# Optimization experiments

Hardware: AMD Instinct MI355X
Metric: run time of the kernel (lower is better)

Reference implementation:

```python
import jax, jax.numpy as jnp
import numpy as np

B, Q, D, H, HD, P = 1, 2048, 2048, 16, 128, 512


def setup_inputs() -> dict:
    key = jax.random.key(0)
    ks = jax.random.split(key, 12)
    x = jax.random.normal(ks[0], (B, Q, D), jnp.float32)
    prefix_key = jax.random.normal(ks[1], (B, P, H, HD), jnp.float32)
    prefix_value = jax.random.normal(ks[2], (B, P, H, HD), jnp.float32)
    s = 1.0 / np.sqrt(D)
    Wq = jax.random.normal(ks[3], (D, H, HD), jnp.float32) * s
    Wk = jax.random.normal(ks[4], (D, H, HD), jnp.float32) * s
    Wv = jax.random.normal(ks[5], (D, H, HD), jnp.float32) * s
    bq = jnp.zeros((H, HD), jnp.float32)
    bk = jnp.zeros((H, HD), jnp.float32)
    bv = jnp.zeros((H, HD), jnp.float32)
    prefix_gate = jax.random.normal(ks[6], (H,), jnp.float32) * 0.1
    Wout = jax.random.normal(ks[7], (H, HD, D), jnp.float32) * (1.0 / np.sqrt(D))
    bout = jnp.zeros((D,), jnp.float32)
    # prefix fully visible, causal mask over the suffix (current sequence)
    causal = jnp.tril(jnp.ones((Q, Q), bool))
    mask = jnp.concatenate([jnp.ones((Q, P), bool), causal], axis=1)[None, None]  # [1,1,Q,P+Q]
    return dict(x=x, prefix_key=prefix_key, prefix_value=prefix_value,
                Wq=Wq, bq=bq, Wk=Wk, bk=bk, Wv=Wv, bv=bv,
                prefix_gate=prefix_gate, Wout=Wout, bout=bout, mask=mask)


def reference(x, prefix_key, prefix_value, Wq, bq, Wk, bk, Wv, bv, prefix_gate, Wout, bout, mask):
    head_dim = Wq.shape[-1]
    pl = prefix_key.shape[1]
    q = jnp.einsum('bqd,dhk->bqhk', x, Wq) + bq   # [B,Q,H,HD]
    k = jnp.einsum('bqd,dhk->bqhk', x, Wk) + bk
    v = jnp.einsum('bqd,dhk->bqhk', x, Wv) + bv
    k = jnp.concatenate([prefix_key, k], axis=1)   # [B,P+Q,H,HD]
    v = jnp.concatenate([prefix_value, v], axis=1)
    q = q / jnp.sqrt(jnp.asarray(head_dim, q.dtype))
    w = jnp.einsum('bqhd,bkhd->bhqk', q, k)        # [B,H,Q,P+Q]
    big_neg = jnp.finfo(w.dtype).min
    w = jnp.where(mask, w, big_neg)
    gate = prefix_gate[None, :, None, None]
    w_prefix = jax.nn.softmax(w[..., :pl]) * gate   # gated prefix segment
    w_suffix = jax.nn.softmax(w[..., pl:])          # regular suffix softmax
    w = jnp.concatenate([w_prefix, w_suffix], axis=-1)
    o = jnp.einsum('bhqk,bkhd->bqhd', w, v)         # [B,Q,H,HD]
    return jnp.einsum('bqhd,hdo->bqo', o, Wout) + bout
```

## Files before the change

### kernel.cpp

```cpp
#include <hip/hip_runtime.h>
#include <hip/hip_bf16.h>

typedef __bf16 bf16x8 __attribute__((ext_vector_type(8)));
typedef __bf16 bf16x4v __attribute__((ext_vector_type(4)));
typedef float f32x4 __attribute__((ext_vector_type(4)));

#define DMODEL 2048
#define NH 16
#define HD 128
#define PLEN 512
#define QLEN 2048
#define KVLEN 2560

__device__ __forceinline__ void gload_lds16(const void* g, void* l) {
  __builtin_amdgcn_global_load_lds((const __attribute__((address_space(1))) void*)g,
                                   (__attribute__((address_space(3))) void*)l, 16, 0, 0);
}


__global__ __launch_bounds__(256) void k_transpose4(const float* __restrict__ s0,
                                                    const float* __restrict__ s1,
                                                    const float* __restrict__ s2,
                                                    const float* __restrict__ s3,
                                                    __bf16* __restrict__ d0,
                                                    __bf16* __restrict__ d1,
                                                    __bf16* __restrict__ d2,
                                                    __bf16* __restrict__ d3) {
  __shared__ float tile[64][65];
  const int z = blockIdx.z;
  const float* in = (z == 0) ? s0 : (z == 1) ? s1 : (z == 2) ? s2 : s3;
  __bf16* out = (z == 0) ? d0 : (z == 1) ? d1 : (z == 2) ? d2 : d3;
  const int t = threadIdx.x;
  const int tx = t & 63, ty = t >> 6;
  const int r0 = blockIdx.y * 64, c0 = blockIdx.x * 64;
#pragma unroll
  for (int i = 0; i < 16; ++i) {
    int r = ty + i * 4;
    tile[r][tx] = in[(size_t)(r0 + r) * DMODEL + c0 + tx];
  }
  __syncthreads();
#pragma unroll
  for (int i = 0; i < 16; ++i) {
    int r = ty + i * 4;
    out[(size_t)(c0 + r) * DMODEL + r0 + tx] = (__bf16)tile[tx][r];
  }
}

__global__ __launch_bounds__(256) void k_f32_to_bf16(const float* __restrict__ in,
                                                     __bf16* __restrict__ out, int n4) {
  int i = blockIdx.x * blockDim.x + threadIdx.x;
  int stride = gridDim.x * blockDim.x;
  for (; i < n4; i += stride) {
    float4 v = ((const float4*)in)[i];
    bf16x4v o;
    o[0] = (__bf16)v.x; o[1] = (__bf16)v.y; o[2] = (__bf16)v.z; o[3] = (__bf16)v.w;
    ((bf16x4v*)out)[i] = o;
  }
}

__global__ __launch_bounds__(256) void k_prefix(const float* __restrict__ pk,
                                                const float* __restrict__ pv,
                                                __bf16* __restrict__ Kall,
                                                __bf16* __restrict__ VT) {
  int idx = blockIdx.x * 256 + threadIdx.x;
  int hd = idx & 127;
  int h = (idx >> 7) & 15;
  int p = idx >> 11;
  Kall[(size_t)h * KVLEN * HD + (size_t)p * HD + hd] = (__bf16)pk[idx];
  VT[(size_t)h * HD * KVLEN + (size_t)hd * KVLEN + p] = (__bf16)pv[idx];
}


template <int BN>
__device__ __forceinline__ void stage_tile(const __bf16* __restrict__ A,
                                           const __bf16* __restrict__ BT,
                                           char* AsmB, char* BsmB,
                                           int m0, int n0, int k0, int w, int l) {
#pragma unroll
  for (int i = 0; i < 2; ++i) {
    int base = i * 4096 + w * 1024;
    int o = base + l * 16;
    int row = o >> 6, col = (o & 63) >> 1;
    gload_lds16(A + (size_t)(m0 + row) * DMODEL + k0 + col, AsmB + base);
  }
  if constexpr (BN == 128) {
#pragma unroll
    for (int i = 0; i < 2; ++i) {
      int base = i * 4096 + w * 1024;
      int o = base + l * 16;
      int row = o >> 6, col = (o & 63) >> 1;
      gload_lds16(BT + (size_t)(n0 + row) * DMODEL + k0 + col, BsmB + base);
    }
  } else {
    int base = w * 1024;
    int o = base + l * 16;
    int row = o >> 6, col = (o & 63) >> 1;
    gload_lds16(BT + (size_t)(n0 + row) * DMODEL + k0 + col, BsmB + base);
  }
}

template <int BN>
__device__ __forceinline__ void gemm_mainloop_db(const __bf16* __restrict__ A,
                                                 const __bf16* __restrict__ BT,
                                                 __bf16* Asm, __bf16* Bsm,
                                                 int m0, int n0, int w, int l,
                                                 f32x4 (&acc)[4][BN / 32]) {
  constexpr int NI = BN / 32;
  constexpr int ABUF = 4096;
  constexpr int BBUF = BN * 32;
  const int lr = l & 15, lg = l >> 4;
  int cur = 0;
  stage_tile<BN>(A, BT, (char*)Asm, (char*)Bsm, m0, n0, 0, w, l);
  __syncthreads();
  for (int k0 = 0; k0 < DMODEL; k0 += 32) {
    if (k0 + 32 < DMODEL)
      stage_tile<BN>(A, BT, (char*)(Asm + (cur ^ 1) * ABUF), (char*)(Bsm + (cur ^ 1) * BBUF),
                     m0, n0, k0 + 32, w, l);
    const __bf16* Ab = Asm + cur * ABUF;
    const __bf16* Bb = Bsm + cur * BBUF;
    bf16x8 af[4], bfv[NI];
#pragma unroll
    for (int mi = 0; mi < 4; ++mi)
      af[mi] = *(const bf16x8*)(Ab + ((w >> 1) * 64 + mi * 16 + lr) * 32 + lg * 8);
#pragma unroll
    for (int ni = 0; ni < NI; ++ni)
      bfv[ni] = *(const bf16x8*)(Bb + ((w & 1) * (BN / 2) + ni * 16 + lr) * 32 + lg * 8);
    __builtin_amdgcn_s_setprio(1);
#pragma unroll
    for (int mi = 0; mi < 4; ++mi)
#pragma unroll
      for (int ni = 0; ni < NI; ++ni)
        acc[mi][ni] = __builtin_amdgcn_mfma_f32_16x16x32_bf16(af[mi], bfv[ni], acc[mi][ni], 0, 0, 0);
    __builtin_amdgcn_s_setprio(0);
    __syncthreads();
    cur ^= 1;
  }
}

__global__ __launch_bounds__(256) void gemm_qkv(const __bf16* __restrict__ xb,
                                                const __bf16* __restrict__ WqT,
                                                const __bf16* __restrict__ WkT,
                                                const __bf16* __restrict__ WvT,
                                                const float* __restrict__ bq,
                                                const float* __restrict__ bk,
                                                const float* __restrict__ bv,
                                                __bf16* __restrict__ Qs,
                                                __bf16* __restrict__ Kall,
                                                __bf16* __restrict__ VT) {
  __shared__ __bf16 Asm[2][4096];
  __shared__ __bf16 Bsm[2][4096];
  const int t = threadIdx.x, w = t >> 6, l = t & 63;
  const int m0 = blockIdx.x * 128, n0 = blockIdx.y * 128;
  const int z = blockIdx.z;
  const __bf16* BT = (z == 0) ? WqT : ((z == 1) ? WkT : WvT);
  const float* bias = (z == 0) ? bq : ((z == 1) ? bk : bv);
  f32x4 acc[4][4];
#pragma unroll
  for (int mi = 0; mi < 4; ++mi)
#pragma unroll
    for (int ni = 0; ni < 4; ++ni) acc[mi][ni] = (f32x4){0.f, 0.f, 0.f, 0.f};
  gemm_mainloop_db<128>(xb, BT, &Asm[0][0], &Bsm[0][0], m0, n0, w, l, acc);
  const int lr = l & 15, lg = l >> 4;
#pragma unroll
  for (int mi = 0; mi < 4; ++mi)
#pragma unroll
    for (int ni = 0; ni < 4; ++ni)
#pragma unroll
      for (int r = 0; r < 4; ++r) {
        int row = m0 + (w >> 1) * 64 + mi * 16 + lg * 4 + r;
        int col = n0 + (w & 1) * 64 + ni * 16 + lr;
        float v = acc[mi][ni][r] + bias[col];
        int hh = col >> 7, hd = col & 127;
        if (z == 0) {
          Qs[(size_t)hh * QLEN * HD + (size_t)row * HD + hd] = (__bf16)(v * 0.08838834764831845f);
        } else if (z == 1) {
          Kall[(size_t)hh * KVLEN * HD + (size_t)(PLEN + row) * HD + hd] = (__bf16)v;
        } else {
          VT[(size_t)hh * HD * KVLEN + (size_t)hd * KVLEN + (PLEN + row)] = (__bf16)v;
        }
      }
}

__global__ __launch_bounds__(256) void gemm_out(const __bf16* __restrict__ Ob,
                                                const __bf16* __restrict__ WoT,
                                                const float* __restrict__ bout,
                                                float* __restrict__ out) {
  __shared__ __bf16 Asm[2][4096];
  __shared__ __bf16 Bsm[2][2048];
  const int t = threadIdx.x, w = t >> 6, l = t & 63;
  const int m0 = blockIdx.x * 128, n0 = blockIdx.y * 64;
  f32x4 acc[4][2];
#pragma unroll
  for (int mi = 0; mi < 4; ++mi)
#pragma unroll
    for (int ni = 0; ni < 2; ++ni) acc[mi][ni] = (f32x4){0.f, 0.f, 0.f, 0.f};
  gemm_mainloop_db<64>(Ob, WoT, &Asm[0][0], &Bsm[0][0], m0, n0, w, l, acc);
  const int lr = l & 15, lg = l >> 4;
#pragma unroll
  for (int mi = 0; mi < 4; ++mi)
#pragma unroll
    for (int ni = 0; ni < 2; ++ni)
#pragma unroll
      for (int r = 0; r < 4; ++r) {
        int row = m0 + (w >> 1) * 64 + mi * 16 + lg * 4 + r;
        int col = n0 + (w & 1) * 32 + ni * 16 + lr;
        out[(size_t)row * DMODEL + col] = acc[mi][ni][r] + bout[col];
      }
}

template <int KS>
__global__ __launch_bounds__(256, 4) void k_attn(const __bf16* __restrict__ Qs,
                                                 const __bf16* __restrict__ Kall,
                                                 const __bf16* __restrict__ VT,
                                                 __bf16* __restrict__ P1buf,
                                                 float* __restrict__ S1buf,
                                                 __bf16* __restrict__ P2buf,
                                                 float* __restrict__ S2buf) {
  __shared__ __bf16 Ksm[2][4096];
  __shared__ __bf16 Vsm[2][4096];
  __shared__ __bf16 Pl[4][16 * 40];
  const int id = blockIdx.x;
  const int b = id & 255, k = id >> 8;
  const int h = b >> 4, m = b & 15;
  int qt, z;
  if constexpr (KS == 2) {
    z = k >> 1;
    const int j = 2 * m + (k >> 1);
    qt = (k & 1) ? (31 - j) : j;
  } else {
    z = 0;
    qt = (k & 1) ? (31 - 2 * m) : (2 * m);
  }
  const int t = threadIdx.x, w = t >> 6, l = t & 63;
  const int lr = l & 15, lg = l >> 4;
  const int q0 = qt * 64 + w * 16;
  const __bf16* Qh = Qs + (size_t)h * QLEN * HD;
  const char* Khb = (const char*)(Kall + (size_t)h * KVLEN * HD);
  const char* Vhb = (const char*)(VT + (size_t)h * HD * KVLEN);
  __bf16* Pw = &Pl[w][0];

  bf16x8 qf[4];
#pragma unroll
  for (int c = 0; c < 4; ++c)
    qf[c] = *(const bf16x8*)(Qh + (size_t)(q0 + lr) * HD + c * 32 + lg * 8);

  f32x4 acc[8];
  float ss[4];

  auto STAGE = [&](int buf, int kb) {
#pragma unroll
    for (int i = 0; i < 2; ++i) {
      int o = (i * 256 + w * 64 + l) * 16;
      int po = o ^ (((o >> 8) & 7) << 4);
      gload_lds16(Khb + (size_t)kb * 256 + po, (char*)&Ksm[buf][0] + i * 4096 + w * 1024);
    }
#pragma unroll
    for (int i = 0; i < 2; ++i) {
      int o = (i * 256 + w * 64 + l) * 16;
      int po = o ^ (((o >> 7) & 7) << 4);
      int row = po >> 6, colb = po & 63;
      gload_lds16(Vhb + (size_t)row * (KVLEN * 2) + (size_t)kb * 2 + colb,
                  (char*)&Vsm[buf][0] + i * 4096 + w * 1024);
    }
  };

  auto COMPUTE = [&](int buf, int mrel, bool domask) {
    const char* Kb = (const char*)&Ksm[buf][0];
    const char* Vb = (const char*)&Vsm[buf][0];
    f32x4 st0 = {0.f, 0.f, 0.f, 0.f}, st1 = {0.f, 0.f, 0.f, 0.f};
    __builtin_amdgcn_s_setprio(1);
#pragma unroll
    for (int c = 0; c < 4; ++c) {
      int o0 = lr * 256 + c * 64 + lg * 16;        o0 ^= ((o0 >> 8) & 7) << 4;
      int o1 = (16 + lr) * 256 + c * 64 + lg * 16; o1 ^= ((o1 >> 8) & 7) << 4;
      bf16x8 kf0 = *(const bf16x8*)(Kb + o0);
      bf16x8 kf1 = *(const bf16x8*)(Kb + o1);
      st0 = __builtin_amdgcn_mfma_f32_16x16x32_bf16(qf[c], kf0, st0, 0, 0, 0);
      st1 = __builtin_amdgcn_mfma_f32_16x16x32_bf16(qf[c], kf1, st1, 0, 0, 0);
    }
    __builtin_amdgcn_s_setprio(0);
#pragma unroll
    for (int r = 0; r < 4; ++r) {
      if (domask) {
        int qq = q0 + lg * 4 + r;
        if (mrel + lr > qq) st0[r] = -1e30f;
        if (mrel + 16 + lr > qq) st1[r] = -1e30f;
      }
      float p0 = __expf(st0[r] - 16.0f);
      float p1 = __expf(st1[r] - 16.0f);
      ss[r] += p0 + p1;
      Pw[(lg * 4 + r) * 40 + lr] = (__bf16)p0;
      Pw[(lg * 4 + r) * 40 + 16 + lr] = (__bf16)p1;
    }
    bf16x8 pf = *(const bf16x8*)(Pw + lr * 40 + lg * 8);
    __builtin_amdgcn_s_setprio(1);
#pragma unroll
    for (int c = 0; c < 8; ++c) {
      int o = (c * 16 + lr) * 64 + lg * 16; o ^= ((o >> 7) & 7) << 4;
      bf16x8 vf = *(const bf16x8*)(Vb + o);
      acc[c] = __builtin_amdgcn_mfma_f32_16x16x32_bf16(pf, vf, acc[c], 0, 0, 0);
    }
    __builtin_amdgcn_s_setprio(0);
  };

  auto STORE_PHASE = [&](__bf16* PBUF, float* SBUF) {
    const size_t rb = (size_t)(z * NH + h) * QLEN;
#pragma unroll
    for (int r = 0; r < 4; ++r) {
      float s = ss[r];
      s += __shfl_xor(s, 1); s += __shfl_xor(s, 2);
      s += __shfl_xor(s, 4); s += __shfl_xor(s, 8);
      const int row = q0 + lg * 4 + r;
      if (lr == 0) SBUF[rb + row] = s;
#pragma unroll
      for (int c = 0; c < 8; ++c)
        PBUF[(rb + row) * HD + c * 16 + lr] = (__bf16)acc[c][r];
    }
  };

#pragma unroll
  for (int c = 0; c < 8; ++c) acc[c] = (f32x4){0.f, 0.f, 0.f, 0.f};
#pragma unroll
  for (int r = 0; r < 4; ++r) ss[r] = 0.f;
  int cur = 0;
  STAGE(0, z * 32);
  __syncthreads();
#pragma unroll 1
  for (int tt = z; tt < 16; tt += KS) {
    if (tt + KS < 16) STAGE(cur ^ 1, (tt + KS) * 32);
    else STAGE(cur ^ 1, PLEN + z * 32);
    COMPUTE(cur, 0, false);
    __syncthreads();
    cur ^= 1;
  }
  STORE_PHASE(P1buf, S1buf);

#pragma unroll
  for (int c = 0; c < 8; ++c) acc[c] = (f32x4){0.f, 0.f, 0.f, 0.f};
#pragma unroll
  for (int r = 0; r < 4; ++r) ss[r] = 0.f;
  const int ntb = 2 * qt + 2;
#pragma unroll 1
  for (int tt = z; tt < ntb; tt += KS) {
    if (tt + KS < ntb) STAGE(cur ^ 1, PLEN + (tt + KS) * 32);
    COMPUTE(cur, tt * 32, tt * 32 + 31 > q0);
    __syncthreads();
    cur ^= 1;
  }
  STORE_PHASE(P2buf, S2buf);
}

template <int KS>
__global__ __launch_bounds__(256) void k_combine(const __bf16* __restrict__ P1buf,
                                                 const float* __restrict__ S1buf,
                                                 const __bf16* __restrict__ P2buf,
                                                 const float* __restrict__ S2buf,
                                                 const float* __restrict__ gate,
                                                 __bf16* __restrict__ Ob) {
  const int idx = blockIdx.x * 256 + threadIdx.x;
  const int d = idx & 127;
  const int q = (idx >> 7) & 2047;
  const int h = idx >> 18;
  const size_t rq = (size_t)h * QLEN + q;
  float a1 = 0.f, a2 = 0.f, s1 = 0.f, s2 = 0.f;
#pragma unroll
  for (int zz = 0; zz < KS; ++zz) {
    const size_t zb = (size_t)zz * NH * QLEN;
    a1 += (float)P1buf[(zb + rq) * HD + d];
    a2 += (float)P2buf[(zb + rq) * HD + d];
    s1 += S1buf[zb + rq];
    s2 += S2buf[zb + rq];
  }
  float o = a1 * (gate[h] / s1) + a2 / s2;
  Ob[(size_t)q * DMODEL + h * HD + d] = (__bf16)o;
}


extern "C" void kernel_launch(void* const* d_in, const int* in_sizes, int n_in,
                              void* d_out, int out_size, void* d_ws, size_t ws_size,
                              hipStream_t stream) {
  const float* x    = (const float*)d_in[0];
  const float* pk   = (const float*)d_in[1];
  const float* pv   = (const float*)d_in[2];
  const float* Wq   = (const float*)d_in[3];
  const float* bq   = (const float*)d_in[4];
  const float* Wk   = (const float*)d_in[5];
  const float* bk   = (const float*)d_in[6];
  const float* Wv   = (const float*)d_in[7];
  const float* bv   = (const float*)d_in[8];
  const float* gate = (const float*)d_in[9];
  const float* Wout = (const float*)d_in[10];
  const float* bout = (const float*)d_in[11];
  float* out = (float*)d_out;

  char* ws = (char*)d_ws;
  size_t off = 0;
  auto alc = [&](size_t bytes) -> char* {
    char* p = ws + off;
    off += bytes;
    off = (off + 255) & ~(size_t)255;
    return p;
  };
  __bf16* xb   = (__bf16*)alc((size_t)DMODEL * DMODEL * 2);
  __bf16* WqT  = (__bf16*)alc((size_t)DMODEL * DMODEL * 2);
  __bf16* WkT  = (__bf16*)alc((size_t)DMODEL * DMODEL * 2);
  __bf16* WvT  = (__bf16*)alc((size_t)DMODEL * DMODEL * 2);
  __bf16* WoT  = (__bf16*)alc((size_t)DMODEL * DMODEL * 2);
  __bf16* Qs   = (__bf16*)alc((size_t)NH * QLEN * HD * 2);
  __bf16* Kall = (__bf16*)alc((size_t)NH * KVLEN * HD * 2);
  __bf16* VTa  = (__bf16*)alc((size_t)NH * HD * KVLEN * 2);
  __bf16* Ob   = (__bf16*)alc((size_t)QLEN * DMODEL * 2);

  const size_t per_split = (size_t)NH * QLEN * HD * 2 * 2
                         + (size_t)NH * QLEN * 4 * 2 + 1024;
  int KS = (off + 2 * per_split <= ws_size) ? 2 : 1;
  __bf16* P1buf = (__bf16*)alc((size_t)KS * NH * QLEN * HD * 2);
  __bf16* P2buf = (__bf16*)alc((size_t)KS * NH * QLEN * HD * 2);
  float*  S1buf = (float*)alc((size_t)KS * NH * QLEN * 4);
  float*  S2buf = (float*)alc((size_t)KS * NH * QLEN * 4);

  k_transpose4<<<dim3(32, 32, 4), 256, 0, stream>>>(Wq, Wk, Wv, Wout, WqT, WkT, WvT, WoT);
  k_f32_to_bf16<<<1024, 256, 0, stream>>>(x, xb, (DMODEL * DMODEL) / 4);
  k_prefix<<<4096, 256, 0, stream>>>(pk, pv, Kall, VTa);

  gemm_qkv<<<dim3(16, 16, 3), 256, 0, stream>>>(xb, WqT, WkT, WvT, bq, bk, bv, Qs, Kall, VTa);

  const int ncomb = (NH * QLEN * HD) / 256;
  if (KS == 2) {
    k_attn<2><<<1024, 256, 0, stream>>>(Qs, Kall, VTa, P1buf, S1buf, P2buf, S2buf);
    k_combine<2><<<ncomb, 256, 0, stream>>>(P1buf, S1buf, P2buf, S2buf, gate, Ob);
  } else {
    k_attn<1><<<512, 256, 0, stream>>>(Qs, Kall, VTa, P1buf, S1buf, P2buf, S2buf);
    k_combine<1><<<ncomb, 256, 0, stream>>>(P1buf, S1buf, P2buf, S2buf, gate, Ob);
  }
  gemm_out<<<dim3(16, 32), 256, 0, stream>>>(Ob, WoT, bout, out);
}
```

Baseline: 195.0 us.

## Fuse prep kernels and keep attention probabilities in registers via transposed QK MFMA

Merges the weight transpose, x conversion and prefix K/V layout kernels into one launch, which removes two kernel launches and their serialization. In the attention kernel the QK^T MFMA operands are swapped so scores arrive transposed. The probability tile is then built with packed bf16 conversion and lane shuffles instead of a round trip through shared memory. The row-sum reduction also shrinks to a single scalar per lane. This removes LDS traffic and per-row shuffle reductions but adds shuffles and selects, and the shuffle index math must exactly match the MFMA operand layout.

```diff
diff --git a/kernel.cpp b/kernel.cpp
--- a/kernel.cpp
+++ b/kernel.cpp
@@ -17,57 +17,64 @@
                                    (__attribute__((address_space(3))) void*)l, 16, 0, 0);
 }
 
-
-__global__ __launch_bounds__(256) void k_transpose4(const float* __restrict__ s0,
-                                                    const float* __restrict__ s1,
-                                                    const float* __restrict__ s2,
-                                                    const float* __restrict__ s3,
-                                                    __bf16* __restrict__ d0,
-                                                    __bf16* __restrict__ d1,
-                                                    __bf16* __restrict__ d2,
-                                                    __bf16* __restrict__ d3) {
+__device__ __forceinline__ unsigned cvt_pk_bf16(float lo, float hi) {
+  unsigned r;
+  asm volatile("v_cvt_pk_bf16_f32 %0, %1, %2" : "=v"(r) : "v"(lo), "v"(hi));
+  return r;
+}
+
+__global__ __launch_bounds__(256) void k_prep(const float* __restrict__ Wq,
+                                              const float* __restrict__ Wk,
+                                              const float* __restrict__ Wv,
+                                              const float* __restrict__ Wo,
+                                              const float* __restrict__ x,
+                                              const float* __restrict__ pk,
+                                              const float* __restrict__ pv,
+                                              __bf16* __restrict__ WqT,
+                                              __bf16* __restrict__ WkT,
+                                              __bf16* __restrict__ WvT,
+                                              __bf16* __restrict__ WoT,
+                                              __bf16* __restrict__ xb,
+                                              __bf16* __restrict__ Kall,
+                                              __bf16* __restrict__ VT) {
   __shared__ float tile[64][65];
   const int z = blockIdx.z;
-  const float* in = (z == 0) ? s0 : (z == 1) ? s1 : (z == 2) ? s2 : s3;
-  __bf16* out = (z == 0) ? d0 : (z == 1) ? d1 : (z == 2) ? d2 : d3;
   const int t = threadIdx.x;
   const int tx = t & 63, ty = t >> 6;
-  const int r0 = blockIdx.y * 64, c0 = blockIdx.x * 64;
-#pragma unroll
-  for (int i = 0; i < 16; ++i) {
-    int r = ty + i * 4;
-    tile[r][tx] = in[(size_t)(r0 + r) * DMODEL + c0 + tx];
-  }
-  __syncthreads();
-#pragma unroll
-  for (int i = 0; i < 16; ++i) {
-    int r = ty + i * 4;
-    out[(size_t)(c0 + r) * DMODEL + r0 + tx] = (__bf16)tile[tx][r];
-  }
-}
-
-__global__ __launch_bounds__(256) void k_f32_to_bf16(const float* __restrict__ in,
-                                                     __bf16* __restrict__ out, int n4) {
-  int i = blockIdx.x * blockDim.x + threadIdx.x;
-  int stride = gridDim.x * blockDim.x;
-  for (; i < n4; i += stride) {
-    float4 v = ((const float4*)in)[i];
-    bf16x4v o;
-    o[0] = (__bf16)v.x; o[1] = (__bf16)v.y; o[2] = (__bf16)v.z; o[3] = (__bf16)v.w;
-    ((bf16x4v*)out)[i] = o;
-  }
-}
-
-__global__ __launch_bounds__(256) void k_prefix(const float* __restrict__ pk,
-                                                const float* __restrict__ pv,
-                                                __bf16* __restrict__ Kall,
-                                                __bf16* __restrict__ VT) {
-  int idx = blockIdx.x * 256 + threadIdx.x;
-  int hd = idx & 127;
-  int h = (idx >> 7) & 15;
-  int p = idx >> 11;
-  Kall[(size_t)h * KVLEN * HD + (size_t)p * HD + hd] = (__bf16)pk[idx];
-  VT[(size_t)h * HD * KVLEN + (size_t)hd * KVLEN + p] = (__bf16)pv[idx];
+  if (z < 4) {
+    const float* in = (z == 0) ? Wq : (z == 1) ? Wk : (z == 2) ? Wv : Wo;
+    __bf16* out = (z == 0) ? WqT : (z == 1) ? WkT : (z == 2) ? WvT : WoT;
+    const int r0 = blockIdx.y * 64, c0 = blockIdx.x * 64;
+#pragma unroll
+    for (int i = 0; i < 16; ++i) {
+      int r = ty + i * 4;
+      tile[r][tx] = in[(size_t)(r0 + r) * DMODEL + c0 + tx];
+    }
+    __syncthreads();
+#pragma unroll
+    for (int i = 0; i < 16; ++i) {
+      int r = ty + i * 4;
+      out[(size_t)(c0 + r) * DMODEL + r0 + tx] = (__bf16)tile[tx][r];
+    }
+  } else if (z == 4) {
+    const int r0 = blockIdx.y * 64, c0 = blockIdx.x * 64;
+#pragma unroll
+    for (int i = 0; i < 16; ++i) {
+      int r = ty + i * 4;
+      xb[(size_t)(r0 + r) * DMODEL + c0 + tx] = (__bf16)x[(size_t)(r0 + r) * DMODEL + c0 + tx];
+    }
+  } else {
+    const int blk = blockIdx.y * 32 + blockIdx.x;
+#pragma unroll
+    for (int i = 0; i < 4; ++i) {
+      int idx = blk * 1024 + i * 256 + t;
+      int hd = idx & 127;
+      int hh = (idx >> 7) & 15;
+      int p = idx >> 11;
+      Kall[(size_t)hh * KVLEN * HD + (size_t)p * HD + hd] = (__bf16)pk[idx];
+      VT[(size_t)hh * HD * KVLEN + (size_t)hd * KVLEN + p] = (__bf16)pv[idx];
+    }
+  }
 }
 
 
@@ -218,7 +225,6 @@
                                                  float* __restrict__ S2buf) {
   __shared__ __bf16 Ksm[2][4096];
   __shared__ __bf16 Vsm[2][4096];
-  __shared__ __bf16 Pl[4][16 * 40];
   const int id = blockIdx.x;
   const int b = id & 255, k = id >> 8;
   const int h = b >> 4, m = b & 15;
@@ -237,7 +243,6 @@
   const __bf16* Qh = Qs + (size_t)h * QLEN * HD;
   const char* Khb = (const char*)(Kall + (size_t)h * KVLEN * HD);
   const char* Vhb = (const char*)(VT + (size_t)h * HD * KVLEN);
-  __bf16* Pw = &Pl[w][0];
 
   bf16x8 qf[4];
 #pragma unroll
@@ -245,7 +250,7 @@
     qf[c] = *(const bf16x8*)(Qh + (size_t)(q0 + lr) * HD + c * 32 + lg * 8);
 
   f32x4 acc[8];
-  float ss[4];
+  float ss;
 
   auto STAGE = [&](int buf, int kb) {
 #pragma unroll
@@ -275,24 +280,40 @@
       int o1 = (16 + lr) * 256 + c * 64 + lg * 16; o1 ^= ((o1 >> 8) & 7) << 4;
       bf16x8 kf0 = *(const bf16x8*)(Kb + o0);
       bf16x8 kf1 = *(const bf16x8*)(Kb + o1);
-      st0 = __builtin_amdgcn_mfma_f32_16x16x32_bf16(qf[c], kf0, st0, 0, 0, 0);
-      st1 = __builtin_amdgcn_mfma_f32_16x16x32_bf16(qf[c], kf1, st1, 0, 0, 0);
+      st0 = __builtin_amdgcn_mfma_f32_16x16x32_bf16(kf0, qf[c], st0, 0, 0, 0);
+      st1 = __builtin_amdgcn_mfma_f32_16x16x32_bf16(kf1, qf[c], st1, 0, 0, 0);
     }
     __builtin_amdgcn_s_setprio(0);
+    const int qabs = q0 + lr;
+    float e0[4], e1[4];
+    float ps = 0.f;
 #pragma unroll
     for (int r = 0; r < 4; ++r) {
+      e0[r] = __expf(st0[r] - 16.0f);
+      e1[r] = __expf(st1[r] - 16.0f);
       if (domask) {
-        int qq = q0 + lg * 4 + r;
-        if (mrel + lr > qq) st0[r] = -1e30f;
-        if (mrel + 16 + lr > qq) st1[r] = -1e30f;
+        if (mrel + 4 * lg + r > qabs) e0[r] = 0.f;
+        if (mrel + 16 + 4 * lg + r > qabs) e1[r] = 0.f;
       }
-      float p0 = __expf(st0[r] - 16.0f);
-      float p1 = __expf(st1[r] - 16.0f);
-      ss[r] += p0 + p1;
-      Pw[(lg * 4 + r) * 40 + lr] = (__bf16)p0;
-      Pw[(lg * 4 + r) * 40 + 16 + lr] = (__bf16)p1;
-    }
-    bf16x8 pf = *(const bf16x8*)(Pw + lr * 40 + lg * 8);
+      ps += e0[r] + e1[r];
+    }
+    ss += ps;
+    unsigned W0 = cvt_pk_bf16(e0[0], e0[1]);
+    unsigned W1 = cvt_pk_bf16(e0[2], e0[3]);
+    unsigned W2 = cvt_pk_bf16(e1[0], e1[1]);
+    unsigned W3 = cvt_pk_bf16(e1[2], e1[3]);
+    const int srcA = lr + (((2 * lg) & 3) << 4);
+    const int srcB = lr + (((2 * lg + 1) & 3) << 4);
+    unsigned A0 = __shfl(W0, srcA), A1 = __shfl(W1, srcA);
+    unsigned A2 = __shfl(W0, srcB), A3 = __shfl(W1, srcB);
+    unsigned B0 = __shfl(W2, srcA), B1 = __shfl(W3, srcA);
+    unsigned B2 = __shfl(W2, srcB), B3 = __shfl(W3, srcB);
+    union { unsigned u[4]; bf16x8 v; } pu;
+    pu.u[0] = (lg < 2) ? A0 : B0;
+    pu.u[1] = (lg < 2) ? A1 : B1;
+    pu.u[2] = (lg < 2) ? A2 : B2;
+    pu.u[3] = (lg < 2) ? A3 : B3;
+    bf16x8 pf = pu.v;
     __builtin_amdgcn_s_setprio(1);
 #pragma unroll
     for (int c = 0; c < 8; ++c) {
@@ -305,13 +326,13 @@
 
   auto STORE_PHASE = [&](__bf16* PBUF, float* SBUF) {
     const size_t rb = (size_t)(z * NH + h) * QLEN;
+    float s = ss;
+    s += __shfl_xor(s, 16);
+    s += __shfl_xor(s, 32);
+    if (l < 16) SBUF[rb + q0 + l] = s;
 #pragma unroll
     for (int r = 0; r < 4; ++r) {
-      float s = ss[r];
-      s += __shfl_xor(s, 1); s += __shfl_xor(s, 2);
-      s += __shfl_xor(s, 4); s += __shfl_xor(s, 8);
       const int row = q0 + lg * 4 + r;
-      if (lr == 0) SBUF[rb + row] = s;
 #pragma unroll
       for (int c = 0; c < 8; ++c)
         PBUF[(rb + row) * HD + c * 16 + lr] = (__bf16)acc[c][r];
@@ -320,8 +341,7 @@
 
 #pragma unroll
   for (int c = 0; c < 8; ++c) acc[c] = (f32x4){0.f, 0.f, 0.f, 0.f};
-#pragma unroll
-  for (int r = 0; r < 4; ++r) ss[r] = 0.f;
+  ss = 0.f;
   int cur = 0;
   STAGE(0, z * 32);
   __syncthreads();
@@ -337,8 +357,7 @@
 
 #pragma unroll
   for (int c = 0; c < 8; ++c) acc[c] = (f32x4){0.f, 0.f, 0.f, 0.f};
-#pragma unroll
-  for (int r = 0; r < 4; ++r) ss[r] = 0.f;
+  ss = 0.f;
   const int ntb = 2 * qt + 2;
 #pragma unroll 1
   for (int tt = z; tt < ntb; tt += KS) {
@@ -419,9 +438,8 @@
   float*  S1buf = (float*)alc((size_t)KS * NH * QLEN * 4);
   float*  S2buf = (float*)alc((size_t)KS * NH * QLEN * 4);
 
-  k_transpose4<<<dim3(32, 32, 4), 256, 0, stream>>>(Wq, Wk, Wv, Wout, WqT, WkT, WvT, WoT);
-  k_f32_to_bf16<<<1024, 256, 0, stream>>>(x, xb, (DMODEL * DMODEL) / 4);
-  k_prefix<<<4096, 256, 0, stream>>>(pk, pv, Kall, VTa);
+  k_prep<<<dim3(32, 32, 6), 256, 0, stream>>>(Wq, Wk, Wv, Wout, x, pk, pv,
+                                              WqT, WkT, WvT, WoT, xb, Kall, VTa);
 
   gemm_qkv<<<dim3(16, 16, 3), 256, 0, stream>>>(xb, WqT, WkT, WvT, bq, bk, bv, Qs, Kall, VTa);
 
```

New measurement: 194.3 us. Within noise of the previous version (-0.3%).
